# Performance work log

Hardware: AMD Instinct MI355X
Metric: run time of the kernel (lower is better)

The kernel has to match this reference:

```python
import jax, jax.numpy as jnp
from jax import lax
import numpy as np

B, H, W, C = 64, 224, 224, 3
OH, OW = 224, 224
EPS = 1e-3  # keras BatchNormalization default epsilon
FLAT = 52 * 52 * 10  # after conv7(valid)->pool2->conv5(valid)->pool2 on 224x224


def setup_inputs() -> dict:
    key = jax.random.key(0)
    ks = jax.random.split(key, 6)
    return {
        "x": jax.random.normal(ks[0], (B, H, W, C), jnp.float32),
        "c1_w": jax.random.normal(ks[1], (7, 7, C, 8), jnp.float32) * 0.05,
        "c1_b": jnp.zeros((8,), jnp.float32),
        "g1": jnp.ones((8,), jnp.float32),
        "b1": jnp.zeros((8,), jnp.float32),
        "m1": jnp.zeros((8,), jnp.float32),
        "v1": jnp.ones((8,), jnp.float32),
        "c2_w": jax.random.normal(ks[2], (5, 5, 8, 10), jnp.float32) * 0.05,
        "c2_b": jnp.zeros((10,), jnp.float32),
        "g2": jnp.ones((10,), jnp.float32),
        "b2": jnp.zeros((10,), jnp.float32),
        "m2": jnp.zeros((10,), jnp.float32),
        "v2": jnp.ones((10,), jnp.float32),
        "d1_w": jax.random.normal(ks[3], (FLAT, 32), jnp.float32) * 0.01,
        "d1_b": jnp.zeros((32,), jnp.float32),
        "d2_w": jax.random.normal(ks[4], (32, 6), jnp.float32) * 0.01,
        "d2_b": jnp.array([1.0, 0.0, 0.0, 0.0, 1.0, 0.0], jnp.float32),  # identity affine
    }


def _conv(x, w, b):
    return lax.conv_general_dilated(x, w, (1, 1), 'VALID',
                                    dimension_numbers=('NHWC', 'HWIO', 'NHWC')) + b


def _maxpool(x):
    return lax.reduce_window(x, -jnp.inf, lax.max, (1, 2, 2, 1), (1, 2, 2, 1), 'VALID')


def _bn(x, g, b, m, v):
    # inference-mode batchnorm: gamma*(x-mean)/sqrt(var+eps)+beta
    return (x - m) * lax.rsqrt(v + EPS) * g + b


def _bilinear(img, px, py):
    # img: [H,W,C]; px,py: [OH,OW] pixel-space sample coords; zero fill outside
    x0 = jnp.floor(px).astype(jnp.int32)
    y0 = jnp.floor(py).astype(jnp.int32)

    def gather(yi, xi):
        valid = (yi >= 0) & (yi < H) & (xi >= 0) & (xi < W)
        v = img[jnp.clip(yi, 0, H - 1), jnp.clip(xi, 0, W - 1)]  # [OH,OW,C]
        return v * valid[..., None]

    wx = (px - x0)[..., None]
    wy = (py - y0)[..., None]
    return (gather(y0, x0) * (1 - wx) * (1 - wy)
            + gather(y0, x0 + 1) * wx * (1 - wy)
            + gather(y0 + 1, x0) * (1 - wx) * wy
            + gather(y0 + 1, x0 + 1) * wx * wy)


def reference(x, c1_w, c1_b, g1, b1, m1, v1, c2_w, c2_b, g2, b2, m2, v2,
              d1_w, d1_b, d2_w, d2_b):
    # localization network
    h = _maxpool(_bn(jax.nn.relu(_conv(x, c1_w, c1_b)), g1, b1, m1, v1))
    h = _maxpool(_bn(jax.nn.relu(_conv(h, c2_w, c2_b)), g2, b2, m2, v2))
    h = h.reshape(h.shape[0], -1)                      # [B, FLAT]
    h = jax.nn.relu(h @ d1_w + d1_b)                   # [B, 32]
    theta = (h @ d2_w + d2_b).reshape(-1, 2, 3)        # [B, 2, 3]

    # normalized homogeneous grid [N,3] with N = OH*OW
    xs = jnp.linspace(-1.0, 1.0, OW)
    ys = jnp.linspace(-1.0, 1.0, OH)
    xg, yg = jnp.meshgrid(xs, ys)
    grid = jnp.stack([xg.ravel(), yg.ravel(), jnp.ones(OH * OW, jnp.float32)], axis=-1)

    coords = jnp.einsum('bij,nj->bni', theta, grid)    # [B, N, 2]
    px = ((coords[..., 0] + 1.0) * 0.5 * (W - 1)).reshape(-1, OH, OW)
    py = ((coords[..., 1] + 1.0) * 0.5 * (H - 1)).reshape(-1, OH, OW)
    return jax.vmap(_bilinear)(x, px, py)              # [B, OH, OW, C]
```

## Files before the change

kernel.cpp:

```cpp
#include <hip/hip_runtime.h>
#include <hip/hip_bf16.h>


#define NCHUNK 423
#define KC 64

__global__ __launch_bounds__(256, 4) void k_conv1(
    const float* __restrict__ x, const float* __restrict__ w,
    const float* __restrict__ bias, const float* __restrict__ g,
    const float* __restrict__ bt, const float* __restrict__ m,
    const float* __restrict__ v, float* __restrict__ out) {
  __shared__ float s_in[2][3][38][42];
  __shared__ float s_bn[3][8];
  const int tid = threadIdx.x;
  const int bx = blockIdx.x, by = blockIdx.y, z = blockIdx.z;
  const int b0 = 2 * z;

  if (tid < 8) {
    float sc = g[tid] * rsqrtf(v[tid] + 1e-3f);
    s_bn[0][tid] = sc;
    s_bn[1][tid] = bt[tid] - m[tid] * sc;
    s_bn[2][tid] = bias[tid];
  }
  const int iy0 = by * 32, ix0 = bx * 32;
  for (int f = tid; f < 2 * 38 * 114; f += 256) {
    int img = f / 4332, rem = f - img * 4332;
    int r = rem / 114, rem2 = rem - r * 114;
    int q = rem2 / 3, c = rem2 - q * 3;
    int gy = iy0 + r; if (gy > 223) gy = 223;
    int gc = ix0 + q; if (gc > 223) gc = 223;
    s_in[img][c][r][q] = x[((size_t)(b0 + img) * 224 + gy) * 224 * 3 + gc * 3 + c];
  }
  __syncthreads();

  const int pxl = tid & 15, pyl = tid >> 4;
  const int lx = 2 * pxl, ly = 2 * pyl;
  float accA[2][2][8], accB[2][2][8];
#pragma unroll
  for (int pr = 0; pr < 2; ++pr)
#pragma unroll
    for (int pc = 0; pc < 2; ++pc)
#pragma unroll
      for (int co = 0; co < 8; ++co) { accA[pr][pc][co] = 0.f; accB[pr][pc][co] = 0.f; }

#pragma unroll 1
  for (int ci = 0; ci < 3; ++ci) {
#pragma unroll 1
    for (int ky = 0; ky < 7; ++ky) {
      float rA[2][8], rB[2][8];
#pragma unroll
      for (int rr = 0; rr < 2; ++rr)
#pragma unroll
        for (int j = 0; j < 4; ++j) {
          float2 ta = *(const float2*)&s_in[0][ci][ly + ky + rr][lx + 2 * j];
          rA[rr][2 * j] = ta.x; rA[rr][2 * j + 1] = ta.y;
          float2 tb = *(const float2*)&s_in[1][ci][ly + ky + rr][lx + 2 * j];
          rB[rr][2 * j] = tb.x; rB[rr][2 * j + 1] = tb.y;
        }
      float wv[7][8];
#pragma unroll
      for (int kx = 0; kx < 7; ++kx) {
        const float* wp = w + ((ky * 7 + kx) * 3 + ci) * 8;
        float4 a = *(const float4*)wp;
        float4 c4 = *(const float4*)(wp + 4);
        wv[kx][0] = a.x;  wv[kx][1] = a.y;  wv[kx][2] = a.z;  wv[kx][3] = a.w;
        wv[kx][4] = c4.x; wv[kx][5] = c4.y; wv[kx][6] = c4.z; wv[kx][7] = c4.w;
      }
#pragma unroll
      for (int kx = 0; kx < 7; ++kx)
#pragma unroll
        for (int pr = 0; pr < 2; ++pr)
#pragma unroll
          for (int pc = 0; pc < 2; ++pc) {
            float ia = rA[pr][kx + pc];
            float ib = rB[pr][kx + pc];
#pragma unroll
            for (int co = 0; co < 8; ++co) {
              accA[pr][pc][co] = fmaf(ia, wv[kx][co], accA[pr][pc][co]);
              accB[pr][pc][co] = fmaf(ib, wv[kx][co], accB[pr][pc][co]);
            }
          }
    }
  }

  const int py = by * 16 + pyl, px = bx * 16 + pxl;
  if (py < 109 && px < 109) {
#pragma unroll
    for (int co = 0; co < 8; ++co) {
      float sc = s_bn[0][co], sh = s_bn[1][co], bs = s_bn[2][co];
      float a0 = fmaxf(accA[0][0][co] + bs, 0.f) * sc + sh;
      float a1 = fmaxf(accA[0][1][co] + bs, 0.f) * sc + sh;
      float a2 = fmaxf(accA[1][0][co] + bs, 0.f) * sc + sh;
      float a3 = fmaxf(accA[1][1][co] + bs, 0.f) * sc + sh;
      out[((size_t)co * 64 + b0) * 109 * 110 + py * 110 + px] =
          fmaxf(fmaxf(a0, a1), fmaxf(a2, a3));
      float c0 = fmaxf(accB[0][0][co] + bs, 0.f) * sc + sh;
      float c1 = fmaxf(accB[0][1][co] + bs, 0.f) * sc + sh;
      float c2 = fmaxf(accB[1][0][co] + bs, 0.f) * sc + sh;
      float c3 = fmaxf(accB[1][1][co] + bs, 0.f) * sc + sh;
      out[((size_t)co * 64 + b0 + 1) * 109 * 110 + py * 110 + px] =
          fmaxf(fmaxf(c0, c1), fmaxf(c2, c3));
    }
  }
}

__global__ __launch_bounds__(256) void k_conv2(
    const float* __restrict__ in, const float* __restrict__ w,
    const float* __restrict__ bias, const float* __restrict__ g,
    const float* __restrict__ bt, const float* __restrict__ m,
    const float* __restrict__ v, float* __restrict__ out) {
  __shared__ float s_in[8][36][38];
  __shared__ float s_bn[3][10];
  const int tid = threadIdx.x;
  const int bx = blockIdx.x, by = blockIdx.y, b = blockIdx.z;

  if (tid < 10) {
    float sc = g[tid] * rsqrtf(v[tid] + 1e-3f);
    s_bn[0][tid] = sc;
    s_bn[1][tid] = bt[tid] - m[tid] * sc;
    s_bn[2][tid] = bias[tid];
  }
  const int iy0 = by * 32, ix0 = bx * 32;
  for (int f = tid; f < 8 * 36 * 36; f += 256) {
    int ci = f / 1296, rem = f - ci * 1296;
    int r = rem / 36, q = rem - r * 36;
    int gy = iy0 + r; if (gy > 108) gy = 108;
    int gc = ix0 + q; if (gc > 108) gc = 108;
    s_in[ci][r][q] = in[(((size_t)ci * 64 + b) * 109 + gy) * 110 + gc];
  }
  __syncthreads();

  const int pxl = tid & 15, pyl = tid >> 4;
  const int lx = 2 * pxl, ly = 2 * pyl;
  float acc[2][2][10];
#pragma unroll
  for (int pr = 0; pr < 2; ++pr)
#pragma unroll
    for (int pc = 0; pc < 2; ++pc)
#pragma unroll
      for (int co = 0; co < 10; ++co) acc[pr][pc][co] = 0.f;

#pragma unroll 1
  for (int ci = 0; ci < 8; ++ci) {
    float rw[6][8];
#pragma unroll
    for (int r = 0; r < 6; ++r)
#pragma unroll
      for (int j = 0; j < 4; ++j) {
        float2 t = *(const float2*)&s_in[ci][ly + r][lx + 2 * j];
        rw[r][2 * j] = t.x; rw[r][2 * j + 1] = t.y;
      }
#pragma unroll
    for (int ky = 0; ky < 5; ++ky) {
      float wv[5][10];
#pragma unroll
      for (int kx = 0; kx < 5; ++kx) {
        const float* wp = w + ((ky * 5 + kx) * 8 + ci) * 10;
#pragma unroll
        for (int u = 0; u < 5; ++u) {
          float2 t = *(const float2*)(wp + 2 * u);
          wv[kx][2 * u] = t.x; wv[kx][2 * u + 1] = t.y;
        }
      }
#pragma unroll
      for (int kx = 0; kx < 5; ++kx)
#pragma unroll
        for (int pr = 0; pr < 2; ++pr)
#pragma unroll
          for (int pc = 0; pc < 2; ++pc) {
            float iv = rw[ky + pr][kx + pc];
#pragma unroll
            for (int co = 0; co < 10; ++co)
              acc[pr][pc][co] = fmaf(iv, wv[kx][co], acc[pr][pc][co]);
          }
    }
  }

  const int py = by * 16 + pyl, px = bx * 16 + pxl;
  if (py < 52 && px < 52) {
    float res[10];
#pragma unroll
    for (int co = 0; co < 10; ++co) {
      float sc = s_bn[0][co], sh = s_bn[1][co], bs = s_bn[2][co];
      float a0 = fmaxf(acc[0][0][co] + bs, 0.f) * sc + sh;
      float a1 = fmaxf(acc[0][1][co] + bs, 0.f) * sc + sh;
      float a2 = fmaxf(acc[1][0][co] + bs, 0.f) * sc + sh;
      float a3 = fmaxf(acc[1][1][co] + bs, 0.f) * sc + sh;
      res[co] = fmaxf(fmaxf(a0, a1), fmaxf(a2, a3));
    }
    float2* op2 = (float2*)&out[(((size_t)b * 52 + py) * 52 + px) * 10];
#pragma unroll
    for (int i = 0; i < 5; i++)
      op2[i] = make_float2(res[2 * i], res[2 * i + 1]);
  }
}

__global__ __launch_bounds__(256) void k_fc1(
    const float* __restrict__ act, const float* __restrict__ w,
    float* __restrict__ partial) {
  __shared__ float s_a[64][KC];
  __shared__ float s_w[KC * 32];
  const int tid = threadIdx.x;
  const int chunk = blockIdx.x;
  const int k0 = chunk * KC;
  for (int f = tid; f < 64 * KC; f += 256) {
    int row = f >> 6, j = f & (KC - 1);
    int k = k0 + j;
    s_a[row][j] = (k < 27040) ? act[(size_t)row * 27040 + k] : 0.f;
  }
  for (int f = tid; f < KC * 32; f += 256) {
    int k = k0 + (f >> 5);
    s_w[f] = (k < 27040) ? w[(size_t)k0 * 32 + f] : 0.f;
  }
  __syncthreads();
  const int o = tid & 31, gg = tid >> 5;
  float sums[8];
#pragma unroll
  for (int i = 0; i < 8; i++) sums[i] = 0.f;
#pragma unroll 2
  for (int j = 0; j < KC; j += 4) {
    float w0 = s_w[j * 32 + o];
    float w1 = s_w[(j + 1) * 32 + o];
    float w2 = s_w[(j + 2) * 32 + o];
    float w3 = s_w[(j + 3) * 32 + o];
#pragma unroll
    for (int i = 0; i < 8; i++) {
      float4 av = *(const float4*)&s_a[gg * 8 + i][j];
      sums[i] = fmaf(av.x, w0, sums[i]);
      sums[i] = fmaf(av.y, w1, sums[i]);
      sums[i] = fmaf(av.z, w2, sums[i]);
      sums[i] = fmaf(av.w, w3, sums[i]);
    }
  }
#pragma unroll
  for (int i = 0; i < 8; i++)
    partial[((size_t)chunk * 64 + gg * 8 + i) * 32 + o] = sums[i];
}

__global__ __launch_bounds__(256) void k_fc2(
    const float* __restrict__ partial, const float* __restrict__ d1b,
    const float* __restrict__ d2w, const float* __restrict__ d2b,
    float* __restrict__ theta) {
  const int b = blockIdx.x;
  const int t = threadIdx.x;
  const int o = t & 31, seg = t >> 5;
  const int c0 = (seg < 7) ? seg * 53 : 371;
  const int cnt = (seg < 7) ? 53 : 52;
  float s = 0.f;
  for (int c = c0; c < c0 + cnt; ++c)
    s += partial[((size_t)c * 64 + b) * 32 + o];
  __shared__ float s_red[8][33];
  s_red[seg][o] = s;
  __syncthreads();
  __shared__ float s_h[32];
  if (t < 32) {
    float tot = 0.f;
#pragma unroll
    for (int sg = 0; sg < 8; ++sg) tot += s_red[sg][t];
    s_h[t] = fmaxf(tot + d1b[t], 0.f);
  }
  __syncthreads();
  if (t < 6) {
    float th = d2b[t];
#pragma unroll
    for (int o2 = 0; o2 < 32; o2++) th = fmaf(s_h[o2], d2w[o2 * 6 + t], th);
    theta[b * 6 + t] = th;
  }
}

__global__ __launch_bounds__(256) void k_sample(
    const float* __restrict__ x, const float* __restrict__ theta,
    float* __restrict__ out) {
  const int b = blockIdx.y;
  __shared__ float th[6];
  if (threadIdx.x < 6) th[threadIdx.x] = theta[b * 6 + threadIdx.x];
  __syncthreads();
  const int t = blockIdx.x * 256 + threadIdx.x;
  const int oy = t / 224, ox = t - oy * 224;
  const float xn = -1.f + (2.f / 223.f) * (float)ox;
  const float yn = -1.f + (2.f / 223.f) * (float)oy;
  const float cx = th[0] * xn + th[1] * yn + th[2];
  const float cy = th[3] * xn + th[4] * yn + th[5];
  const float px = (cx + 1.f) * 0.5f * 223.f;
  const float py = (cy + 1.f) * 0.5f * 223.f;
  const float x0f = floorf(px), y0f = floorf(py);
  const int x0 = (int)x0f, y0 = (int)y0f;
  const float wx = px - x0f, wy = py - y0f;
  const float* xb = x + (size_t)b * 224 * 224 * 3;
  float a0 = 0.f, a1 = 0.f, a2 = 0.f;
#pragma unroll
  for (int dy = 0; dy < 2; dy++) {
    const int yi = y0 + dy;
    const bool vy = (yi >= 0) && (yi < 224);
    const int yc = yi < 0 ? 0 : (yi > 223 ? 223 : yi);
    const float wyv = dy ? wy : 1.f - wy;
#pragma unroll
    for (int dx = 0; dx < 2; dx++) {
      const int xi = x0 + dx;
      const bool vx = (xi >= 0) && (xi < 224);
      const int xc = xi < 0 ? 0 : (xi > 223 ? 223 : xi);
      const float wv = wyv * (dx ? wx : 1.f - wx) * ((vx && vy) ? 1.f : 0.f);
      const float* p = &xb[(yc * 224 + xc) * 3];
      a0 = fmaf(p[0], wv, a0);
      a1 = fmaf(p[1], wv, a1);
      a2 = fmaf(p[2], wv, a2);
    }
  }
  float* op = &out[((size_t)b * 50176 + t) * 3];
  op[0] = a0; op[1] = a1; op[2] = a2;
}

extern "C" void kernel_launch(void* const* d_in, const int* in_sizes, int n_in,
                              void* d_out, int out_size, void* d_ws, size_t ws_size,
                              hipStream_t stream) {
  const float* x    = (const float*)d_in[0];
  const float* c1w  = (const float*)d_in[1];
  const float* c1b  = (const float*)d_in[2];
  const float* g1   = (const float*)d_in[3];
  const float* b1   = (const float*)d_in[4];
  const float* m1   = (const float*)d_in[5];
  const float* v1   = (const float*)d_in[6];
  const float* c2w  = (const float*)d_in[7];
  const float* c2b  = (const float*)d_in[8];
  const float* g2   = (const float*)d_in[9];
  const float* b2   = (const float*)d_in[10];
  const float* m2   = (const float*)d_in[11];
  const float* v2   = (const float*)d_in[12];
  const float* d1w  = (const float*)d_in[13];
  const float* d1b  = (const float*)d_in[14];
  const float* d2w  = (const float*)d_in[15];
  const float* d2b  = (const float*)d_in[16];
  float* out = (float*)d_out;

  float* ws = (float*)d_ws;
  float* p1    = ws;
  float* p2    = p1 + 6138880;
  float* theta = p2 + 1730560;
  float* part  = ws;

  k_conv1<<<dim3(7, 7, 32), 256, 0, stream>>>(x, c1w, c1b, g1, b1, m1, v1, p1);
  k_conv2<<<dim3(4, 4, 64), 256, 0, stream>>>(p1, c2w, c2b, g2, b2, m2, v2, p2);
  k_fc1<<<NCHUNK, 256, 0, stream>>>(p2, d1w, part);
  k_fc2<<<64, 256, 0, stream>>>(part, d1b, d2w, d2b, theta);
  k_sample<<<dim3(196, 64), 256, 0, stream>>>(x, theta, out);
}
```

Before: 299.3 us.

## Process one image per conv1 block with register-cached rows and split launches

Conv1 now handles a single image per block instead of two. That halves the shared tile and the accumulator registers, and the launch bound rises to 8 blocks per SM. Each thread loads all 8 input rows once per input channel into registers and fully unrolls the ky loop, so the per-ky shared-memory reloads go away. The grid is split into four launches of 16 images each through a new zbase argument. This trades weight reuse across two images for higher occupancy, and adds launch overhead plus register pressure from the 64-float row cache.

Result: slower. 328.3 us (+9.7%).

```diff
diff --git a/kernel.cpp b/kernel.cpp
--- a/kernel.cpp
+++ b/kernel.cpp
@@ -5,16 +5,15 @@
 #define NCHUNK 423
 #define KC 64
 
-__global__ __launch_bounds__(256, 4) void k_conv1(
+__global__ __launch_bounds__(256, 8) void k_conv1(
     const float* __restrict__ x, const float* __restrict__ w,
     const float* __restrict__ bias, const float* __restrict__ g,
     const float* __restrict__ bt, const float* __restrict__ m,
-    const float* __restrict__ v, float* __restrict__ out) {
-  __shared__ float s_in[2][3][38][42];
+    const float* __restrict__ v, float* __restrict__ out, int zbase) {
+  __shared__ float s_in[3][38][42];
   __shared__ float s_bn[3][8];
   const int tid = threadIdx.x;
-  const int bx = blockIdx.x, by = blockIdx.y, z = blockIdx.z;
-  const int b0 = 2 * z;
+  const int bx = blockIdx.x, by = blockIdx.y, b = zbase + blockIdx.z;
 
   if (tid < 8) {
     float sc = g[tid] * rsqrtf(v[tid] + 1e-3f);
@@ -23,40 +22,38 @@
     s_bn[2][tid] = bias[tid];
   }
   const int iy0 = by * 32, ix0 = bx * 32;
-  for (int f = tid; f < 2 * 38 * 114; f += 256) {
-    int img = f / 4332, rem = f - img * 4332;
-    int r = rem / 114, rem2 = rem - r * 114;
-    int q = rem2 / 3, c = rem2 - q * 3;
+  const float* xb = x + (size_t)b * 224 * 224 * 3;
+  for (int f = tid; f < 38 * 114; f += 256) {
+    int r = f / 114, rem = f - r * 114;
+    int q = rem / 3, c = rem - q * 3;
     int gy = iy0 + r; if (gy > 223) gy = 223;
     int gc = ix0 + q; if (gc > 223) gc = 223;
-    s_in[img][c][r][q] = x[((size_t)(b0 + img) * 224 + gy) * 224 * 3 + gc * 3 + c];
+    s_in[c][r][q] = xb[(gy * 224 + gc) * 3 + c];
   }
   __syncthreads();
 
   const int pxl = tid & 15, pyl = tid >> 4;
   const int lx = 2 * pxl, ly = 2 * pyl;
-  float accA[2][2][8], accB[2][2][8];
+  float acc[2][2][8];
 #pragma unroll
   for (int pr = 0; pr < 2; ++pr)
 #pragma unroll
     for (int pc = 0; pc < 2; ++pc)
 #pragma unroll
-      for (int co = 0; co < 8; ++co) { accA[pr][pc][co] = 0.f; accB[pr][pc][co] = 0.f; }
+      for (int co = 0; co < 8; ++co) acc[pr][pc][co] = 0.f;
 
 #pragma unroll 1
   for (int ci = 0; ci < 3; ++ci) {
-#pragma unroll 1
+    float rw[8][8];
+#pragma unroll
+    for (int r = 0; r < 8; ++r)
+#pragma unroll
+      for (int j = 0; j < 4; ++j) {
+        float2 t = *(const float2*)&s_in[ci][ly + r][lx + 2 * j];
+        rw[r][2 * j] = t.x; rw[r][2 * j + 1] = t.y;
+      }
+#pragma unroll
     for (int ky = 0; ky < 7; ++ky) {
-      float rA[2][8], rB[2][8];
-#pragma unroll
-      for (int rr = 0; rr < 2; ++rr)
-#pragma unroll
-        for (int j = 0; j < 4; ++j) {
-          float2 ta = *(const float2*)&s_in[0][ci][ly + ky + rr][lx + 2 * j];
-          rA[rr][2 * j] = ta.x; rA[rr][2 * j + 1] = ta.y;
-          float2 tb = *(const float2*)&s_in[1][ci][ly + ky + rr][lx + 2 * j];
-          rB[rr][2 * j] = tb.x; rB[rr][2 * j + 1] = tb.y;
-        }
       float wv[7][8];
 #pragma unroll
       for (int kx = 0; kx < 7; ++kx) {
@@ -72,13 +69,10 @@
         for (int pr = 0; pr < 2; ++pr)
 #pragma unroll
           for (int pc = 0; pc < 2; ++pc) {
-            float ia = rA[pr][kx + pc];
-            float ib = rB[pr][kx + pc];
-#pragma unroll
-            for (int co = 0; co < 8; ++co) {
-              accA[pr][pc][co] = fmaf(ia, wv[kx][co], accA[pr][pc][co]);
-              accB[pr][pc][co] = fmaf(ib, wv[kx][co], accB[pr][pc][co]);
-            }
+            float iv = rw[ky + pr][kx + pc];
+#pragma unroll
+            for (int co = 0; co < 8; ++co)
+              acc[pr][pc][co] = fmaf(iv, wv[kx][co], acc[pr][pc][co]);
           }
     }
   }
@@ -88,18 +82,12 @@
 #pragma unroll
     for (int co = 0; co < 8; ++co) {
       float sc = s_bn[0][co], sh = s_bn[1][co], bs = s_bn[2][co];
-      float a0 = fmaxf(accA[0][0][co] + bs, 0.f) * sc + sh;
-      float a1 = fmaxf(accA[0][1][co] + bs, 0.f) * sc + sh;
-      float a2 = fmaxf(accA[1][0][co] + bs, 0.f) * sc + sh;
-      float a3 = fmaxf(accA[1][1][co] + bs, 0.f) * sc + sh;
-      out[((size_t)co * 64 + b0) * 109 * 110 + py * 110 + px] =
+      float a0 = fmaxf(acc[0][0][co] + bs, 0.f) * sc + sh;
+      float a1 = fmaxf(acc[0][1][co] + bs, 0.f) * sc + sh;
+      float a2 = fmaxf(acc[1][0][co] + bs, 0.f) * sc + sh;
+      float a3 = fmaxf(acc[1][1][co] + bs, 0.f) * sc + sh;
+      out[((size_t)co * 64 + b) * 109 * 110 + py * 110 + px] =
           fmaxf(fmaxf(a0, a1), fmaxf(a2, a3));
-      float c0 = fmaxf(accB[0][0][co] + bs, 0.f) * sc + sh;
-      float c1 = fmaxf(accB[0][1][co] + bs, 0.f) * sc + sh;
-      float c2 = fmaxf(accB[1][0][co] + bs, 0.f) * sc + sh;
-      float c3 = fmaxf(accB[1][1][co] + bs, 0.f) * sc + sh;
-      out[((size_t)co * 64 + b0 + 1) * 109 * 110 + py * 110 + px] =
-          fmaxf(fmaxf(c0, c1), fmaxf(c2, c3));
     }
   }
 }
@@ -338,7 +326,8 @@
   float* theta = p2 + 1730560;
   float* part  = ws;
 
-  k_conv1<<<dim3(7, 7, 32), 256, 0, stream>>>(x, c1w, c1b, g1, b1, m1, v1, p1);
+  for (int zb = 0; zb < 64; zb += 16)
+    k_conv1<<<dim3(7, 7, 16), 256, 0, stream>>>(x, c1w, c1b, g1, b1, m1, v1, p1, zb);
   k_conv2<<<dim3(4, 4, 64), 256, 0, stream>>>(p1, c2w, c2b, g2, b2, m2, v2, p2);
   k_fc1<<<NCHUNK, 256, 0, stream>>>(p2, d1w, part);
   k_fc2<<<64, 256, 0, stream>>>(part, d1b, d2w, d2b, theta);
```
